# Kernel tuning notes

Hardware: AMD Instinct MI355X
Metric: run time of the kernel (lower is better)

## Reference

```python
import jax, jax.numpy as jnp
import numpy as np

B, T, N, D = 16, 64, 22, 64
K, E, DT, H = 4, 8, 5, 64
KL_WEIGHT = 0.01


def setup_inputs() -> dict:
    key = jax.random.key(0)
    ks = jax.random.split(key, 4)
    x = jax.random.normal(ks[0], (B, T, N, D), jnp.float32)
    # fixed-degree neighbor table: joint j's neighbors are (j..j+3) mod N, self first
    nb = jnp.asarray((np.arange(N)[:, None] + np.arange(K)[None, :]) % N, jnp.int32)
    Fin = DT * K * D  # 1280 flattened local window feature
    W1 = jax.random.normal(ks[1], (N, E, Fin, H), jnp.float32) / np.float32(np.sqrt(Fin))
    b1 = jnp.zeros((N, E, H), jnp.float32)
    W2 = jax.random.normal(ks[2], (N, E, H, H), jnp.float32) / np.float32(np.sqrt(H))
    b2 = jnp.zeros((N, E, H), jnp.float32)
    W3 = jax.random.normal(ks[3], (N, E, H, D), jnp.float32) / np.float32(np.sqrt(H))
    b3 = jnp.zeros((N, E, D), jnp.float32)
    return {"x": x, "nb": nb, "W1": W1, "b1": b1, "W2": W2, "b2": b2, "W3": W3, "b3": b3}


def reference(x, nb, W1, b1, W2, b2, W3, b3):
    Bx, Tx, Nx, Dx = x.shape
    dt_half = DT // 2
    # all valid centers t in range(dt_half, T - dt_half - 1), batched (no python loop over t, j)
    ts = jnp.arange(dt_half, Tx - dt_half - 1)            # [Tw]
    offs = jnp.arange(-dt_half, dt_half + 1)              # [DT]
    win = x[:, ts[:, None] + offs[None, :]]               # [B,Tw,DT,N,D]
    dx = win[:, :, :, nb, :]                              # [B,Tw,DT,N,K,D] neighbor gather
    Tw = ts.shape[0]
    f = dx.transpose(0, 1, 3, 2, 4, 5).reshape(Bx, Tw, Nx, DT * K * Dx)  # [B,Tw,N,Fin]
    # per-joint per-expert MLP, fully batched
    h = jax.nn.relu(jnp.einsum('btnf,nefh->btneh', f, W1) + b1)
    h = jax.nn.relu(jnp.einsum('btneh,nehg->btneg', h, W2) + b2)
    pred = jnp.einsum('btneh,nehd->btned', h, W3) + b3    # [B,Tw,N,E,D]
    y = x[:, ts]                                          # [B,Tw,N,D] center-frame target
    err = jnp.mean((pred - y[:, :, :, None, :]) ** 2, axis=-1)  # [B,Tw,N,E]
    min_err = jnp.min(err, axis=-1)                       # winner-take-all (monopoly)
    expert_idx_all = jnp.argmin(err, axis=-1)             # [B,Tw,N]
    p = jax.nn.softmax(-err, axis=-1)
    kl = jnp.sum(p * (jnp.log(p + 1e-9) + jnp.log(jnp.float32(E))), axis=-1)  # KL to uniform
    per_tj = jnp.mean(min_err + KL_WEIGHT * kl, axis=0)   # [Tw,N] batch-mean local losses
    # original divides by the FINAL loop indices j and t (off-by-one kept for fidelity)
    total = jnp.sum(per_tj) / jnp.float32(Nx - 1) / jnp.float32(Tx - dt_half - 2)
    expert_idx = expert_idx_all[:, -1, -1]                # last (t, j) iteration, [B]
    return total, expert_idx
```

## Files before the change

### kernel.cpp

```cpp
#include <hip/hip_runtime.h>
#include <math.h>

#define B_   16
#define T_   64
#define N_   22
#define D_   64
#define K_   4
#define E_   8
#define H_   64
#define TW   59
#define M_   (B_ * TW)
#define NE_  (N_ * E_)
#define NDXT (N_ * D_)
#define XTOT (B_ * T_ * N_ * D_)

typedef __attribute__((ext_vector_type(8))) short short8;
typedef __attribute__((ext_vector_type(4))) float float4v;

#define ERRWS_BYTES  ((size_t)(M_ * N_ * E_) * 4)
#define XH_OFF       (ERRWS_BYTES)

__device__ inline unsigned rtn_bf16(float f) {
    unsigned u = __float_as_uint(f);
    return (u + 0x7fffu + ((u >> 16) & 1u)) >> 16;
}

__global__ __launch_bounds__(256) void xtrunc_kernel(
    const float* __restrict__ x, short* __restrict__ xh, float* __restrict__ out)
{
    if (blockIdx.x == 0 && threadIdx.x == 0) out[0] = 0.f;
    int i = (blockIdx.x * 256 + threadIdx.x) * 4;
    if (i >= XTOT) return;
    float4 v = *(const float4*)(x + i);
    uint2 hp;
    hp.x = rtn_bf16(v.x) | (rtn_bf16(v.y) << 16);
    hp.y = rtn_bf16(v.z) | (rtn_bf16(v.w) << 16);
    *(uint2*)(xh + i) = hp;
}

__global__ __launch_bounds__(256, 4) void moe_err_kernel(
    const float* __restrict__ x, const short* __restrict__ xh,
    const int* __restrict__ nb,
    const float* __restrict__ W1, const float* __restrict__ W2,
    const float* __restrict__ W3,
    const float* __restrict__ b1, const float* __restrict__ b2,
    const float* __restrict__ b3, float* __restrict__ err_ws)
{
    const int tid = threadIdx.x;
    const int w   = tid >> 6;
    const int L   = tid & 63;
    const int g   = blockIdx.x;
    const int e   = g & 7;
    const int mt  = (g >> 3) & 7;
    const int n   = g >> 6;
    const int ne  = n * E_ + e;

    __shared__ __align__(16) char smem[26624];
    char*  wbuf   = smem;
    short* himg   = (short*)(smem + 8192);

    const int lrow = L & 15;
    const int dseg = (L >> 4) * 8;
    const int ccol = L & 15;
    const int qrow = (L >> 4) * 4;
    const int rowbase = mt * 128 + w * 32;

    const short* xhrow[2];
    #pragma unroll
    for (int rt = 0; rt < 2; ++rt) {
        int m  = rowbase + rt * 16 + lrow;
        int mc = m < M_ ? m : M_ - 1;
        int b = mc / TW, t = mc % TW;
        xhrow[rt] = xh + (size_t)(b * T_ + t) * NDXT;
    }

    const int o0 = __builtin_amdgcn_readfirstlane(nb[n * K_ + 0]) * D_;
    const int o1 = __builtin_amdgcn_readfirstlane(nb[n * K_ + 1]) * D_;
    const int o2 = __builtin_amdgcn_readfirstlane(nb[n * K_ + 2]) * D_;
    const int o3 = __builtin_amdgcn_readfirstlane(nb[n * K_ + 3]) * D_;

    const float* W1ne = W1 + (size_t)ne * (1280 * 64);
    const float* W2ne = W2 + (size_t)ne * 4096;
    const float* W3ne = W3 + (size_t)ne * 4096;
    auto csrc = [&](int c) {
        return c < 20 ? (W1ne + (size_t)c * 4096) : (c == 20 ? W2ne : W3ne);
    };

    float wf[2][2][8];
    uint4 wph[2];
    auto loadWf = [&](int wb, const float* src) {
        #pragma unroll
        for (int p = 0; p < 2; ++p) {
            const int pi = 2 * w + p;
            const float* sp = src + ((pi >> 2) * 32 + (L >> 4) * 8) * 64
                                  + ((pi & 3) * 16 + (L & 15));
            #pragma unroll
            for (int j = 0; j < 8; ++j) wf[wb][p][j] = sp[j * 64];
        }
    };
    auto packW = [&](int wb) {
        #pragma unroll
        for (int p = 0; p < 2; ++p) {
            unsigned hs[8];
            #pragma unroll
            for (int j = 0; j < 8; ++j) hs[j] = rtn_bf16(wf[wb][p][j]);
            wph[p].x = hs[0] | (hs[1] << 16); wph[p].y = hs[2] | (hs[3] << 16);
            wph[p].z = hs[4] | (hs[5] << 16); wph[p].w = hs[6] | (hs[7] << 16);
        }
    };
    auto storeW = [&]() {
        #pragma unroll
        for (int p = 0; p < 2; ++p) {
            *(uint4*)(wbuf + (size_t)(2 * w + p) * 1024 + (size_t)L * 16) = wph[p];
        }
    };
    auto bfrag = [&](int s2, int cf) -> short8 {
        return *(const short8*)(wbuf + (size_t)(s2 * 4 + cf) * 1024
                                     + (size_t)L * 16);
    };

    loadWf(0, csrc(0));
    loadWf(1, csrc(1));
    packW(0);

    float4v acc1[2][4];
    #pragma unroll
    for (int rt = 0; rt < 2; ++rt)
        #pragma unroll
        for (int cf = 0; cf < 4; ++cf) acc1[rt][cf] = (float4v)0.f;

    for (int dt = 0; dt < 5; ++dt) {
        #pragma unroll
        for (int kk = 0; kk < 4; ++kk) {
            const int c = dt * 4 + kk;
            __syncthreads();
            storeW();
            __syncthreads();

            loadWf(c & 1, csrc(c + 2));

            const int okk = (kk == 0) ? o0 : ((kk == 1) ? o1 : ((kk == 2) ? o2 : o3));
            const int off = dt * NDXT + okk;

            short8 ah[2][2];
            #pragma unroll
            for (int s2 = 0; s2 < 2; ++s2)
                #pragma unroll
                for (int rt = 0; rt < 2; ++rt)
                    ah[s2][rt] = *(const short8*)(xhrow[rt] + off + s2 * 32 + dseg);

            #pragma unroll
            for (int s2 = 0; s2 < 2; ++s2)
                #pragma unroll
                for (int cf = 0; cf < 4; ++cf) {
                    short8 bh = bfrag(s2, cf);
                    #pragma unroll
                    for (int rt = 0; rt < 2; ++rt)
                        acc1[rt][cf] = __builtin_amdgcn_mfma_f32_16x16x32_bf16(ah[s2][rt], bh, acc1[rt][cf], 0, 0, 0);
                }
            packW((c + 1) & 1);
        }
    }

    __syncthreads();
    storeW();
    #pragma unroll
    for (int cf = 0; cf < 4; ++cf) {
        float bv = b1[(size_t)ne * H_ + cf * 16 + ccol];
        #pragma unroll
        for (int rt = 0; rt < 2; ++rt)
            #pragma unroll
            for (int reg = 0; reg < 4; ++reg) {
                float hv = fmaxf(acc1[rt][cf][reg] + bv, 0.f);
                himg[(w * 32 + rt * 16 + qrow + reg) * 72 + cf * 16 + ccol] =
                    (short)rtn_bf16(hv);
            }
    }
    __syncthreads();

    float4v acc2[2][4];
    #pragma unroll
    for (int rt = 0; rt < 2; ++rt)
        #pragma unroll
        for (int cf = 0; cf < 4; ++cf) acc2[rt][cf] = (float4v)0.f;
    #pragma unroll
    for (int s2 = 0; s2 < 2; ++s2) {
        short8 ha[2];
        #pragma unroll
        for (int rt = 0; rt < 2; ++rt)
            ha[rt] = *(const short8*)&himg[(w * 32 + rt * 16 + lrow) * 72 + s2 * 32 + dseg];
        #pragma unroll
        for (int cf = 0; cf < 4; ++cf) {
            short8 bh = bfrag(s2, cf);
            #pragma unroll
            for (int rt = 0; rt < 2; ++rt)
                acc2[rt][cf] = __builtin_amdgcn_mfma_f32_16x16x32_bf16(ha[rt], bh, acc2[rt][cf], 0, 0, 0);
        }
    }
    packW(1);

    __syncthreads();
    storeW();
    #pragma unroll
    for (int cf = 0; cf < 4; ++cf) {
        float bv = b2[(size_t)ne * H_ + cf * 16 + ccol];
        #pragma unroll
        for (int rt = 0; rt < 2; ++rt)
            #pragma unroll
            for (int reg = 0; reg < 4; ++reg) {
                float hv = fmaxf(acc2[rt][cf][reg] + bv, 0.f);
                himg[(w * 32 + rt * 16 + qrow + reg) * 72 + cf * 16 + ccol] =
                    (short)rtn_bf16(hv);
            }
    }
    __syncthreads();

    float4v acc3[2][4];
    #pragma unroll
    for (int rt = 0; rt < 2; ++rt)
        #pragma unroll
        for (int cf = 0; cf < 4; ++cf) acc3[rt][cf] = (float4v)0.f;
    #pragma unroll
    for (int s2 = 0; s2 < 2; ++s2) {
        short8 ha[2];
        #pragma unroll
        for (int rt = 0; rt < 2; ++rt)
            ha[rt] = *(const short8*)&himg[(w * 32 + rt * 16 + lrow) * 72 + s2 * 32 + dseg];
        #pragma unroll
        for (int cf = 0; cf < 4; ++cf) {
            short8 bh = bfrag(s2, cf);
            #pragma unroll
            for (int rt = 0; rt < 2; ++rt)
                acc3[rt][cf] = __builtin_amdgcn_mfma_f32_16x16x32_bf16(ha[rt], bh, acc3[rt][cf], 0, 0, 0);
        }
    }

    {
        float b3v[4];
        #pragma unroll
        for (int cf = 0; cf < 4; ++cf) b3v[cf] = b3[(size_t)ne * D_ + cf * 16 + ccol];

        #pragma unroll
        for (int rt = 0; rt < 2; ++rt) {
            #pragma unroll
            for (int reg = 0; reg < 4; ++reg) {
                const int m  = rowbase + rt * 16 + qrow + reg;
                const int mc = m < M_ ? m : M_ - 1;
                const int b = mc / TW, t = mc % TW;
                const float* yp = x + ((size_t)(b * T_ + t + 2) * N_ + n) * D_;
                float s = 0.f;
                #pragma unroll
                for (int cf = 0; cf < 4; ++cf) {
                    float d = acc3[rt][cf][reg] + b3v[cf] - yp[cf * 16 + ccol];
                    s += d * d;
                }
                s += __shfl_xor(s, 1);
                s += __shfl_xor(s, 2);
                s += __shfl_xor(s, 4);
                s += __shfl_xor(s, 8);
                if (ccol == 0 && m < M_) {
                    err_ws[((size_t)m * N_ + n) * E_ + e] = s * (1.f / 64.f);
                }
            }
        }
    }
}

__global__ __launch_bounds__(256) void fix_kernel(
    const float* __restrict__ x, const int* __restrict__ nb,
    const float* __restrict__ W1, const float* __restrict__ b1,
    const float* __restrict__ W2, const float* __restrict__ b2,
    const float* __restrict__ W3, const float* __restrict__ b3,
    float* __restrict__ err_ws)
{
    const int b = blockIdx.x >> 3;
    const int e = blockIdx.x & 7;
    const int n = N_ - 1;
    const int t = TW - 1;
    const int ne = n * E_ + e;
    const int j = threadIdx.x & 63;
    const int q = threadIdx.x >> 6;

    __shared__ float fbuf[1280];
    __shared__ float part[4][64];
    __shared__ float h1s[64];
    __shared__ float h2s[64];

    for (int i = threadIdx.x; i < 1280; i += 256) {
        int dt = i >> 8, r = i & 255;
        int k = r >> 6, d = r & 63;
        int nk = nb[n * K_ + k];
        fbuf[i] = x[(((size_t)(b * T_ + t + dt)) * N_ + nk) * D_ + d];
    }
    __syncthreads();

    const float* W1p = W1 + (size_t)ne * 1280 * 64;
    float s = 0.f;
    #pragma unroll 8
    for (int k = q * 320; k < q * 320 + 320; ++k) s += fbuf[k] * W1p[(size_t)k * 64 + j];
    part[q][j] = s;
    __syncthreads();
    if (q == 0)
        h1s[j] = fmaxf(part[0][j] + part[1][j] + part[2][j] + part[3][j]
                       + b1[(size_t)ne * H_ + j], 0.f);
    __syncthreads();

    const float* W2p = W2 + (size_t)ne * 4096;
    s = 0.f;
    #pragma unroll
    for (int k = q * 16; k < q * 16 + 16; ++k) s += h1s[k] * W2p[k * 64 + j];
    part[q][j] = s;
    __syncthreads();
    if (q == 0)
        h2s[j] = fmaxf(part[0][j] + part[1][j] + part[2][j] + part[3][j]
                       + b2[(size_t)ne * H_ + j], 0.f);
    __syncthreads();

    const float* W3p = W3 + (size_t)ne * 4096;
    s = 0.f;
    #pragma unroll
    for (int k = q * 16; k < q * 16 + 16; ++k) s += h2s[k] * W3p[k * 64 + j];
    part[q][j] = s;
    __syncthreads();
    if (q == 0) {
        float pred = part[0][j] + part[1][j] + part[2][j] + part[3][j]
                   + b3[(size_t)ne * D_ + j];
        float y = x[(((size_t)(b * T_ + t + 2)) * N_ + n) * D_ + j];
        float d = pred - y;
        float sq = d * d;
        sq += __shfl_xor(sq, 1);
        sq += __shfl_xor(sq, 2);
        sq += __shfl_xor(sq, 4);
        sq += __shfl_xor(sq, 8);
        sq += __shfl_xor(sq, 16);
        sq += __shfl_xor(sq, 32);
        if (j == 0) {
            int m = b * TW + t;
            err_ws[((size_t)m * N_ + n) * E_ + e] = sq * (1.f / 64.f);
        }
    }
}

__global__ __launch_bounds__(256) void moe_reduce_kernel(
    const float* __restrict__ err_ws, float* __restrict__ out)
{
    const int tid = threadIdx.x;
    const int idx = blockIdx.x * 256 + tid;
    float v = 0.f;
    if (idx < M_ * N_) {
        const int m = idx / N_, n = idx % N_;
        const float* ep = err_ws + (size_t)idx * E_;
        float ev[E_];
        float4 e0 = *(const float4*)ep;
        float4 e1 = *(const float4*)(ep + 4);
        ev[0] = e0.x; ev[1] = e0.y; ev[2] = e0.z; ev[3] = e0.w;
        ev[4] = e1.x; ev[5] = e1.y; ev[6] = e1.z; ev[7] = e1.w;
        float mn = ev[0];
        int am = 0;
        #pragma unroll
        for (int i = 1; i < E_; ++i) {
            if (ev[i] < mn) { mn = ev[i]; am = i; }
        }
        float p[E_];
        float Z = 0.f;
        #pragma unroll
        for (int i = 0; i < E_; ++i) { p[i] = expf(mn - ev[i]); Z += p[i]; }
        const float invZ = 1.f / Z;
        float kl = 0.f;
        #pragma unroll
        for (int i = 0; i < E_; ++i) {
            float q = p[i] * invZ;
            kl += q * (logf(q + 1e-9f) + 2.0794415416798357f);
        }
        v = mn + 0.01f * kl;
        const int t = m % TW, b = m / TW;
        if (t == TW - 1 && n == N_ - 1) out[1 + b] = (float)am;
    }
    __shared__ float sd[256];
    sd[tid] = v;
    __syncthreads();
    for (int s = 128; s > 0; s >>= 1) {
        if (tid < s) sd[tid] += sd[tid + s];
        __syncthreads();
    }
    if (tid == 0) atomicAdd(out, sd[0] * (1.f / 20160.f));
}

extern "C" void kernel_launch(void* const* d_in, const int* in_sizes, int n_in,
                              void* d_out, int out_size, void* d_ws, size_t ws_size,
                              hipStream_t stream)
{
    const float* x  = (const float*)d_in[0];
    const int*   nb = (const int*)d_in[1];
    const float* W1 = (const float*)d_in[2];
    const float* b1 = (const float*)d_in[3];
    const float* W2 = (const float*)d_in[4];
    const float* b2 = (const float*)d_in[5];
    const float* W3 = (const float*)d_in[6];
    const float* b3 = (const float*)d_in[7];
    float* out    = (float*)d_out;
    float* err_ws = (float*)d_ws;
    short* xh     = (short*)((char*)d_ws + XH_OFF);

    hipLaunchKernelGGL(xtrunc_kernel, dim3((XTOT / 4 + 255) / 256), dim3(256), 0, stream,
                       x, xh, out);
    hipLaunchKernelGGL(moe_err_kernel, dim3(NE_ * 8), dim3(256), 0, stream,
                       x, xh, nb, W1, W2, W3, b1, b2, b3, err_ws);
    hipLaunchKernelGGL(fix_kernel, dim3(B_ * E_), dim3(256), 0, stream,
                       x, nb, W1, b1, W2, b2, W3, b3, err_ws);
    const int nred = (M_ * N_ + 255) / 256;
    hipLaunchKernelGGL(moe_reduce_kernel, dim3(nred), dim3(256), 0, stream, err_ws, out);
}
```

Baseline: 204.7 us.

## Fuse fix and bf16 pre-pass, fold reduction into last block, prefetch A

Merges the bf16 conversion of x and the special-case fix computation into one pre-kernel, so the main kernel no longer overwrites that entry. The final softmax/KL reduction moves into the main kernel using an atomic counter, letting the last-finishing block do it. This cuts the launch count from four to two. The A-fragment global loads are double-buffered one step ahead of the MFMAs to hide latency. The tail reduction now runs on a single block, which serializes that work, and it uses the fast exp/log intrinsics.

```diff
diff --git a/kernel.cpp b/kernel.cpp
--- a/kernel.cpp
+++ b/kernel.cpp
@@ -11,31 +11,118 @@
 #define TW   59
 #define M_   (B_ * TW)
 #define NE_  (N_ * E_)
+#define GRID (NE_ * 8)
 #define NDXT (N_ * D_)
 #define XTOT (B_ * T_ * N_ * D_)
+#define NF4  (XTOT / 4)
 
 typedef __attribute__((ext_vector_type(8))) short short8;
 typedef __attribute__((ext_vector_type(4))) float float4v;
 
 #define ERRWS_BYTES  ((size_t)(M_ * N_ * E_) * 4)
 #define XH_OFF       (ERRWS_BYTES)
+#define XIMG_BYTES   ((size_t)XTOT * 2)
+#define CNT_OFF      (XH_OFF + XIMG_BYTES)
 
 __device__ inline unsigned rtn_bf16(float f) {
     unsigned u = __float_as_uint(f);
     return (u + 0x7fffu + ((u >> 16) & 1u)) >> 16;
 }
 
-__global__ __launch_bounds__(256) void xtrunc_kernel(
-    const float* __restrict__ x, short* __restrict__ xh, float* __restrict__ out)
+__global__ __launch_bounds__(256) void pre_kernel(
+    const float* __restrict__ x, const int* __restrict__ nb,
+    const float* __restrict__ W1, const float* __restrict__ b1,
+    const float* __restrict__ W2, const float* __restrict__ b2,
+    const float* __restrict__ W3, const float* __restrict__ b3,
+    float* __restrict__ err_ws, short* __restrict__ xh,
+    unsigned* __restrict__ cnt)
 {
-    if (blockIdx.x == 0 && threadIdx.x == 0) out[0] = 0.f;
-    int i = (blockIdx.x * 256 + threadIdx.x) * 4;
-    if (i >= XTOT) return;
-    float4 v = *(const float4*)(x + i);
-    uint2 hp;
-    hp.x = rtn_bf16(v.x) | (rtn_bf16(v.y) << 16);
-    hp.y = rtn_bf16(v.z) | (rtn_bf16(v.w) << 16);
-    *(uint2*)(xh + i) = hp;
+    const int g   = blockIdx.x;
+    const int tid = threadIdx.x;
+    __shared__ __align__(16) char smem[6656];
+
+    if (g < 128) {
+        const int b = g >> 3;
+        const int e = g & 7;
+        const int n = N_ - 1, t = TW - 1;
+        const int ne = n * E_ + e;
+        const int j = tid & 63;
+        const int q = tid >> 6;
+
+        float* fbuf = (float*)smem;
+        float (*part)[64] = (float(*)[64])(smem + 5120);
+        float* h1s = (float*)(smem + 6144);
+        float* h2s = (float*)(smem + 6400);
+
+        if (g == 0 && tid == 0) *cnt = 0u;
+
+        for (int i = tid; i < 1280; i += 256) {
+            int dt = i >> 8, r = i & 255;
+            int k = r >> 6, d = r & 63;
+            int nk = nb[n * K_ + k];
+            fbuf[i] = x[(((size_t)(b * T_ + t + dt)) * N_ + nk) * D_ + d];
+        }
+        __syncthreads();
+
+        const float* W1p = W1 + (size_t)ne * 1280 * 64;
+        float s = 0.f;
+        #pragma unroll 8
+        for (int k = q * 320; k < q * 320 + 320; ++k) s += fbuf[k] * W1p[(size_t)k * 64 + j];
+        part[q][j] = s;
+        __syncthreads();
+        if (q == 0)
+            h1s[j] = fmaxf(part[0][j] + part[1][j] + part[2][j] + part[3][j]
+                           + b1[(size_t)ne * H_ + j], 0.f);
+        __syncthreads();
+
+        const float* W2p = W2 + (size_t)ne * 4096;
+        s = 0.f;
+        #pragma unroll
+        for (int k = q * 16; k < q * 16 + 16; ++k) s += h1s[k] * W2p[k * 64 + j];
+        part[q][j] = s;
+        __syncthreads();
+        if (q == 0)
+            h2s[j] = fmaxf(part[0][j] + part[1][j] + part[2][j] + part[3][j]
+                           + b2[(size_t)ne * H_ + j], 0.f);
+        __syncthreads();
+
+        const float* W3p = W3 + (size_t)ne * 4096;
+        s = 0.f;
+        #pragma unroll
+        for (int k = q * 16; k < q * 16 + 16; ++k) s += h2s[k] * W3p[k * 64 + j];
+        part[q][j] = s;
+        __syncthreads();
+        if (q == 0) {
+            float pred = part[0][j] + part[1][j] + part[2][j] + part[3][j]
+                       + b3[(size_t)ne * D_ + j];
+            float y = x[(((size_t)(b * T_ + t + 2)) * N_ + n) * D_ + j];
+            float d = pred - y;
+            float sq = d * d;
+            sq += __shfl_xor(sq, 1);
+            sq += __shfl_xor(sq, 2);
+            sq += __shfl_xor(sq, 4);
+            sq += __shfl_xor(sq, 8);
+            sq += __shfl_xor(sq, 16);
+            sq += __shfl_xor(sq, 32);
+            if (j == 0) {
+                int m = b * TW + t;
+                err_ws[((size_t)m * N_ + n) * E_ + e] = sq * (1.f / 64.f);
+            }
+        }
+    } else {
+        int base = (g - 128) * 256 + tid;
+        #pragma unroll
+        for (int it = 0; it < 2; ++it) {
+            int i = base + it * (1280 * 256);
+            if (i < NF4) {
+                float4 v = *(const float4*)(x + (size_t)i * 4);
+                uint2 hp;
+                hp.x = rtn_bf16(v.x) | (rtn_bf16(v.y) << 16);
+                hp.y = rtn_bf16(v.z) | (rtn_bf16(v.w) << 16);
+                *(uint2*)(xh + (size_t)i * 4) = hp;
+            }
+        }
+    }
 }
 
 __global__ __launch_bounds__(256, 4) void moe_err_kernel(
@@ -44,7 +131,8 @@
     const float* __restrict__ W1, const float* __restrict__ W2,
     const float* __restrict__ W3,
     const float* __restrict__ b1, const float* __restrict__ b2,
-    const float* __restrict__ b3, float* __restrict__ err_ws)
+    const float* __restrict__ b3, float* __restrict__ err_ws,
+    unsigned* __restrict__ cnt, float* __restrict__ out)
 {
     const int tid = threadIdx.x;
     const int w   = tid >> 6;
@@ -56,8 +144,8 @@
     const int ne  = n * E_ + e;
 
     __shared__ __align__(16) char smem[26624];
-    char*  wbuf   = smem;
-    short* himg   = (short*)(smem + 8192);
+    char*  wbuf = smem;
+    short* himg = (short*)(smem + 8192);
 
     const int lrow = L & 15;
     const int dseg = (L >> 4) * 8;
@@ -110,17 +198,26 @@
     };
     auto storeW = [&]() {
         #pragma unroll
-        for (int p = 0; p < 2; ++p) {
+        for (int p = 0; p < 2; ++p)
             *(uint4*)(wbuf + (size_t)(2 * w + p) * 1024 + (size_t)L * 16) = wph[p];
-        }
     };
     auto bfrag = [&](int s2, int cf) -> short8 {
         return *(const short8*)(wbuf + (size_t)(s2 * 4 + cf) * 1024
                                      + (size_t)L * 16);
     };
 
+    short8 ahb[2][2][2];
+    auto loadA = [&](int off, int buf) {
+        #pragma unroll
+        for (int s2 = 0; s2 < 2; ++s2)
+            #pragma unroll
+            for (int rt = 0; rt < 2; ++rt)
+                ahb[buf][s2][rt] = *(const short8*)(xhrow[rt] + off + s2 * 32 + dseg);
+    };
+
     loadWf(0, csrc(0));
     loadWf(1, csrc(1));
+    loadA(o0, 0);
     packW(0);
 
     float4v acc1[2][4];
@@ -137,17 +234,12 @@
             storeW();
             __syncthreads();
 
-            loadWf(c & 1, csrc(c + 2));
-
-            const int okk = (kk == 0) ? o0 : ((kk == 1) ? o1 : ((kk == 2) ? o2 : o3));
-            const int off = dt * NDXT + okk;
-
-            short8 ah[2][2];
-            #pragma unroll
-            for (int s2 = 0; s2 < 2; ++s2)
-                #pragma unroll
-                for (int rt = 0; rt < 2; ++rt)
-                    ah[s2][rt] = *(const short8*)(xhrow[rt] + off + s2 * 32 + dseg);
+            loadWf(kk & 1, csrc(c + 2));
+            if (c < 19) {
+                const int dtn = (kk == 3) ? dt + 1 : dt;
+                const int okn = (kk == 0) ? o1 : ((kk == 1) ? o2 : ((kk == 2) ? o3 : o0));
+                loadA(dtn * NDXT + okn, (kk + 1) & 1);
+            }
 
             #pragma unroll
             for (int s2 = 0; s2 < 2; ++s2)
@@ -156,7 +248,7 @@
                     short8 bh = bfrag(s2, cf);
                     #pragma unroll
                     for (int rt = 0; rt < 2; ++rt)
-                        acc1[rt][cf] = __builtin_amdgcn_mfma_f32_16x16x32_bf16(ah[s2][rt], bh, acc1[rt][cf], 0, 0, 0);
+                        acc1[rt][cf] = __builtin_amdgcn_mfma_f32_16x16x32_bf16(ahb[kk & 1][s2][rt], bh, acc1[rt][cf], 0, 0, 0);
                 }
             packW((c + 1) & 1);
         }
@@ -258,132 +350,61 @@
                 s += __shfl_xor(s, 2);
                 s += __shfl_xor(s, 4);
                 s += __shfl_xor(s, 8);
-                if (ccol == 0 && m < M_) {
+                if (ccol == 0 && m < M_ && !(n == N_ - 1 && t == TW - 1)) {
                     err_ws[((size_t)m * N_ + n) * E_ + e] = s * (1.f / 64.f);
                 }
             }
         }
     }
-}
-
-__global__ __launch_bounds__(256) void fix_kernel(
-    const float* __restrict__ x, const int* __restrict__ nb,
-    const float* __restrict__ W1, const float* __restrict__ b1,
-    const float* __restrict__ W2, const float* __restrict__ b2,
-    const float* __restrict__ W3, const float* __restrict__ b3,
-    float* __restrict__ err_ws)
-{
-    const int b = blockIdx.x >> 3;
-    const int e = blockIdx.x & 7;
-    const int n = N_ - 1;
-    const int t = TW - 1;
-    const int ne = n * E_ + e;
-    const int j = threadIdx.x & 63;
-    const int q = threadIdx.x >> 6;
-
-    __shared__ float fbuf[1280];
-    __shared__ float part[4][64];
-    __shared__ float h1s[64];
-    __shared__ float h2s[64];
-
-    for (int i = threadIdx.x; i < 1280; i += 256) {
-        int dt = i >> 8, r = i & 255;
-        int k = r >> 6, d = r & 63;
-        int nk = nb[n * K_ + k];
-        fbuf[i] = x[(((size_t)(b * T_ + t + dt)) * N_ + nk) * D_ + d];
-    }
-    __syncthreads();
-
-    const float* W1p = W1 + (size_t)ne * 1280 * 64;
-    float s = 0.f;
-    #pragma unroll 8
-    for (int k = q * 320; k < q * 320 + 320; ++k) s += fbuf[k] * W1p[(size_t)k * 64 + j];
-    part[q][j] = s;
-    __syncthreads();
-    if (q == 0)
-        h1s[j] = fmaxf(part[0][j] + part[1][j] + part[2][j] + part[3][j]
-                       + b1[(size_t)ne * H_ + j], 0.f);
-    __syncthreads();
-
-    const float* W2p = W2 + (size_t)ne * 4096;
-    s = 0.f;
-    #pragma unroll
-    for (int k = q * 16; k < q * 16 + 16; ++k) s += h1s[k] * W2p[k * 64 + j];
-    part[q][j] = s;
-    __syncthreads();
-    if (q == 0)
-        h2s[j] = fmaxf(part[0][j] + part[1][j] + part[2][j] + part[3][j]
-                       + b2[(size_t)ne * H_ + j], 0.f);
-    __syncthreads();
-
-    const float* W3p = W3 + (size_t)ne * 4096;
-    s = 0.f;
-    #pragma unroll
-    for (int k = q * 16; k < q * 16 + 16; ++k) s += h2s[k] * W3p[k * 64 + j];
-    part[q][j] = s;
-    __syncthreads();
-    if (q == 0) {
-        float pred = part[0][j] + part[1][j] + part[2][j] + part[3][j]
-                   + b3[(size_t)ne * D_ + j];
-        float y = x[(((size_t)(b * T_ + t + 2)) * N_ + n) * D_ + j];
-        float d = pred - y;
-        float sq = d * d;
-        sq += __shfl_xor(sq, 1);
-        sq += __shfl_xor(sq, 2);
-        sq += __shfl_xor(sq, 4);
-        sq += __shfl_xor(sq, 8);
-        sq += __shfl_xor(sq, 16);
-        sq += __shfl_xor(sq, 32);
-        if (j == 0) {
-            int m = b * TW + t;
-            err_ws[((size_t)m * N_ + n) * E_ + e] = sq * (1.f / 64.f);
-        }
-    }
-}
-
-__global__ __launch_bounds__(256) void moe_reduce_kernel(
-    const float* __restrict__ err_ws, float* __restrict__ out)
-{
-    const int tid = threadIdx.x;
-    const int idx = blockIdx.x * 256 + tid;
-    float v = 0.f;
-    if (idx < M_ * N_) {
-        const int m = idx / N_, n = idx % N_;
-        const float* ep = err_ws + (size_t)idx * E_;
-        float ev[E_];
-        float4 e0 = *(const float4*)ep;
-        float4 e1 = *(const float4*)(ep + 4);
-        ev[0] = e0.x; ev[1] = e0.y; ev[2] = e0.z; ev[3] = e0.w;
-        ev[4] = e1.x; ev[5] = e1.y; ev[6] = e1.z; ev[7] = e1.w;
-        float mn = ev[0];
-        int am = 0;
-        #pragma unroll
-        for (int i = 1; i < E_; ++i) {
-            if (ev[i] < mn) { mn = ev[i]; am = i; }
-        }
-        float p[E_];
-        float Z = 0.f;
-        #pragma unroll
-        for (int i = 0; i < E_; ++i) { p[i] = expf(mn - ev[i]); Z += p[i]; }
-        const float invZ = 1.f / Z;
-        float kl = 0.f;
-        #pragma unroll
-        for (int i = 0; i < E_; ++i) {
-            float q = p[i] * invZ;
-            kl += q * (logf(q + 1e-9f) + 2.0794415416798357f);
-        }
-        v = mn + 0.01f * kl;
-        const int t = m % TW, b = m / TW;
-        if (t == TW - 1 && n == N_ - 1) out[1 + b] = (float)am;
-    }
-    __shared__ float sd[256];
-    sd[tid] = v;
-    __syncthreads();
-    for (int s = 128; s > 0; s >>= 1) {
-        if (tid < s) sd[tid] += sd[tid + s];
-        __syncthreads();
-    }
-    if (tid == 0) atomicAdd(out, sd[0] * (1.f / 20160.f));
+
+    __syncthreads();
+    if (tid == 0) {
+        __threadfence();
+        unsigned old = atomicAdd(cnt, 1u);
+        *(int*)(smem + 1024) = (old == (unsigned)(GRID - 1)) ? 1 : 0;
+    }
+    __syncthreads();
+    if (*(int*)(smem + 1024)) {
+        __threadfence();
+        float partial = 0.f;
+        for (int idx = tid; idx < M_ * N_; idx += 256) {
+            const int m = idx / N_, nn = idx % N_;
+            const float* ep = err_ws + (size_t)idx * E_;
+            float ev[E_];
+            float4 e0 = *(const float4*)ep;
+            float4 e1 = *(const float4*)(ep + 4);
+            ev[0] = e0.x; ev[1] = e0.y; ev[2] = e0.z; ev[3] = e0.w;
+            ev[4] = e1.x; ev[5] = e1.y; ev[6] = e1.z; ev[7] = e1.w;
+            float mn = ev[0];
+            int am = 0;
+            #pragma unroll
+            for (int i = 1; i < E_; ++i) {
+                if (ev[i] < mn) { mn = ev[i]; am = i; }
+            }
+            float p[E_];
+            float Z = 0.f;
+            #pragma unroll
+            for (int i = 0; i < E_; ++i) { p[i] = __expf(mn - ev[i]); Z += p[i]; }
+            const float invZ = 1.f / Z;
+            float kl = 0.f;
+            #pragma unroll
+            for (int i = 0; i < E_; ++i) {
+                float q = p[i] * invZ;
+                kl += q * (__logf(q + 1e-9f) + 2.0794415416798357f);
+            }
+            partial += mn + 0.01f * kl;
+            const int t = m % TW, b = m / TW;
+            if (t == TW - 1 && nn == N_ - 1) out[1 + b] = (float)am;
+        }
+        float* sd = (float*)smem;
+        sd[tid] = partial;
+        __syncthreads();
+        for (int s = 128; s > 0; s >>= 1) {
+            if (tid < s) sd[tid] += sd[tid + s];
+            __syncthreads();
+        }
+        if (tid == 0) out[0] = sd[0] * (1.f / 20160.f);
+    }
 }
 
 extern "C" void kernel_launch(void* const* d_in, const int* in_sizes, int n_in,
@@ -401,13 +422,10 @@
     float* out    = (float*)d_out;
     float* err_ws = (float*)d_ws;
     short* xh     = (short*)((char*)d_ws + XH_OFF);
-
-    hipLaunchKernelGGL(xtrunc_kernel, dim3((XTOT / 4 + 255) / 256), dim3(256), 0, stream,
-                       x, xh, out);
-    hipLaunchKernelGGL(moe_err_kernel, dim3(NE_ * 8), dim3(256), 0, stream,
-                       x, xh, nb, W1, W2, W3, b1, b2, b3, err_ws);
-    hipLaunchKernelGGL(fix_kernel, dim3(B_ * E_), dim3(256), 0, stream,
-                       x, nb, W1, b1, W2, b2, W3, b3, err_ws);
-    const int nred = (M_ * N_ + 255) / 256;
-    hipLaunchKernelGGL(moe_reduce_kernel, dim3(nred), dim3(256), 0, stream, err_ws, out);
+    unsigned* cnt = (unsigned*)((char*)d_ws + CNT_OFF);
+
+    hipLaunchKernelGGL(pre_kernel, dim3(GRID), dim3(256), 0, stream,
+                       x, nb, W1, b1, W2, b2, W3, b3, err_ws, xh, cnt);
+    hipLaunchKernelGGL(moe_err_kernel, dim3(GRID), dim3(256), 0, stream,
+                       x, xh, nb, W1, W2, W3, b1, b2, b3, err_ws, cnt, out);
 }
```

Result: slower. 318.3 us (+55.5%).

## Fuse fp32 fix-up and bf16 conversion into one pre-kernel, raise occupancy

Applied to the files above, without the earlier changes.

Merges the separate bf16 truncation kernel and the fp32 fix-up kernel for the last (t, n) position into a single pre-kernel. The first 128 blocks do the fp32 fix-up and the remaining blocks convert x to bf16 with two elements per thread. The main MoE kernel now skips writing the fix-up entries, so ordering between the two kernels no longer matters. This removes one launch and lets the fix-up run beside the conversion instead of after the main kernel. Launch bounds on the main kernel are raised from 4 to 6 waves, which can cause register pressure or spills.

```diff
diff --git a/kernel.cpp b/kernel.cpp
--- a/kernel.cpp
+++ b/kernel.cpp
@@ -11,8 +11,10 @@
 #define TW   59
 #define M_   (B_ * TW)
 #define NE_  (N_ * E_)
+#define GRID (NE_ * 8)
 #define NDXT (N_ * D_)
 #define XTOT (B_ * T_ * N_ * D_)
+#define NF4  (XTOT / 4)
 
 typedef __attribute__((ext_vector_type(8))) short short8;
 typedef __attribute__((ext_vector_type(4))) float float4v;
@@ -25,20 +27,103 @@
     return (u + 0x7fffu + ((u >> 16) & 1u)) >> 16;
 }
 
-__global__ __launch_bounds__(256) void xtrunc_kernel(
-    const float* __restrict__ x, short* __restrict__ xh, float* __restrict__ out)
+__global__ __launch_bounds__(256) void pre_kernel(
+    const float* __restrict__ x, const int* __restrict__ nb,
+    const float* __restrict__ W1, const float* __restrict__ b1,
+    const float* __restrict__ W2, const float* __restrict__ b2,
+    const float* __restrict__ W3, const float* __restrict__ b3,
+    float* __restrict__ err_ws, short* __restrict__ xh,
+    float* __restrict__ out)
 {
-    if (blockIdx.x == 0 && threadIdx.x == 0) out[0] = 0.f;
-    int i = (blockIdx.x * 256 + threadIdx.x) * 4;
-    if (i >= XTOT) return;
-    float4 v = *(const float4*)(x + i);
-    uint2 hp;
-    hp.x = rtn_bf16(v.x) | (rtn_bf16(v.y) << 16);
-    hp.y = rtn_bf16(v.z) | (rtn_bf16(v.w) << 16);
-    *(uint2*)(xh + i) = hp;
+    const int g   = blockIdx.x;
+    const int tid = threadIdx.x;
+    __shared__ __align__(16) char smem[6656];
+
+    if (g < 128) {
+        const int b = g >> 3;
+        const int e = g & 7;
+        const int n = N_ - 1, t = TW - 1;
+        const int ne = n * E_ + e;
+        const int j = tid & 63;
+        const int q = tid >> 6;
+
+        float* fbuf = (float*)smem;
+        float (*part)[64] = (float(*)[64])(smem + 5120);
+        float* h1s = (float*)(smem + 6144);
+        float* h2s = (float*)(smem + 6400);
+
+        if (g == 0 && tid == 0) out[0] = 0.f;
+
+        for (int i = tid; i < 1280; i += 256) {
+            int dt = i >> 8, r = i & 255;
+            int k = r >> 6, d = r & 63;
+            int nk = nb[n * K_ + k];
+            fbuf[i] = x[(((size_t)(b * T_ + t + dt)) * N_ + nk) * D_ + d];
+        }
+        __syncthreads();
+
+        const float* W1p = W1 + (size_t)ne * 1280 * 64;
+        float s = 0.f;
+        #pragma unroll 8
+        for (int k = q * 320; k < q * 320 + 320; ++k) s += fbuf[k] * W1p[(size_t)k * 64 + j];
+        part[q][j] = s;
+        __syncthreads();
+        if (q == 0)
+            h1s[j] = fmaxf(part[0][j] + part[1][j] + part[2][j] + part[3][j]
+                           + b1[(size_t)ne * H_ + j], 0.f);
+        __syncthreads();
+
+        const float* W2p = W2 + (size_t)ne * 4096;
+        s = 0.f;
+        #pragma unroll
+        for (int k = q * 16; k < q * 16 + 16; ++k) s += h1s[k] * W2p[k * 64 + j];
+        part[q][j] = s;
+        __syncthreads();
+        if (q == 0)
+            h2s[j] = fmaxf(part[0][j] + part[1][j] + part[2][j] + part[3][j]
+                           + b2[(size_t)ne * H_ + j], 0.f);
+        __syncthreads();
+
+        const float* W3p = W3 + (size_t)ne * 4096;
+        s = 0.f;
+        #pragma unroll
+        for (int k = q * 16; k < q * 16 + 16; ++k) s += h2s[k] * W3p[k * 64 + j];
+        part[q][j] = s;
+        __syncthreads();
+        if (q == 0) {
+            float pred = part[0][j] + part[1][j] + part[2][j] + part[3][j]
+                       + b3[(size_t)ne * D_ + j];
+            float y = x[(((size_t)(b * T_ + t + 2)) * N_ + n) * D_ + j];
+            float d = pred - y;
+            float sq = d * d;
+            sq += __shfl_xor(sq, 1);
+            sq += __shfl_xor(sq, 2);
+            sq += __shfl_xor(sq, 4);
+            sq += __shfl_xor(sq, 8);
+            sq += __shfl_xor(sq, 16);
+            sq += __shfl_xor(sq, 32);
+            if (j == 0) {
+                int m = b * TW + t;
+                err_ws[((size_t)m * N_ + n) * E_ + e] = sq * (1.f / 64.f);
+            }
+        }
+    } else {
+        int base = (g - 128) * 256 + tid;
+        #pragma unroll
+        for (int it = 0; it < 2; ++it) {
+            int i = base + it * (1280 * 256);
+            if (i < NF4) {
+                float4 v = *(const float4*)(x + (size_t)i * 4);
+                uint2 hp;
+                hp.x = rtn_bf16(v.x) | (rtn_bf16(v.y) << 16);
+                hp.y = rtn_bf16(v.z) | (rtn_bf16(v.w) << 16);
+                *(uint2*)(xh + (size_t)i * 4) = hp;
+            }
+        }
+    }
 }
 
-__global__ __launch_bounds__(256, 4) void moe_err_kernel(
+__global__ __launch_bounds__(256, 6) void moe_err_kernel(
     const float* __restrict__ x, const short* __restrict__ xh,
     const int* __restrict__ nb,
     const float* __restrict__ W1, const float* __restrict__ W2,
@@ -56,8 +141,8 @@
     const int ne  = n * E_ + e;
 
     __shared__ __align__(16) char smem[26624];
-    char*  wbuf   = smem;
-    short* himg   = (short*)(smem + 8192);
+    char*  wbuf = smem;
+    short* himg = (short*)(smem + 8192);
 
     const int lrow = L & 15;
     const int dseg = (L >> 4) * 8;
@@ -110,9 +195,8 @@
     };
     auto storeW = [&]() {
         #pragma unroll
-        for (int p = 0; p < 2; ++p) {
+        for (int p = 0; p < 2; ++p)
             *(uint4*)(wbuf + (size_t)(2 * w + p) * 1024 + (size_t)L * 16) = wph[p];
-        }
     };
     auto bfrag = [&](int s2, int cf) -> short8 {
         return *(const short8*)(wbuf + (size_t)(s2 * 4 + cf) * 1024
@@ -258,85 +342,10 @@
                 s += __shfl_xor(s, 2);
                 s += __shfl_xor(s, 4);
                 s += __shfl_xor(s, 8);
-                if (ccol == 0 && m < M_) {
+                if (ccol == 0 && m < M_ && !(n == N_ - 1 && t == TW - 1)) {
                     err_ws[((size_t)m * N_ + n) * E_ + e] = s * (1.f / 64.f);
                 }
             }
-        }
-    }
-}
-
-__global__ __launch_bounds__(256) void fix_kernel(
-    const float* __restrict__ x, const int* __restrict__ nb,
-    const float* __restrict__ W1, const float* __restrict__ b1,
-    const float* __restrict__ W2, const float* __restrict__ b2,
-    const float* __restrict__ W3, const float* __restrict__ b3,
-    float* __restrict__ err_ws)
-{
-    const int b = blockIdx.x >> 3;
-    const int e = blockIdx.x & 7;
-    const int n = N_ - 1;
-    const int t = TW - 1;
-    const int ne = n * E_ + e;
-    const int j = threadIdx.x & 63;
-    const int q = threadIdx.x >> 6;
-
-    __shared__ float fbuf[1280];
-    __shared__ float part[4][64];
-    __shared__ float h1s[64];
-    __shared__ float h2s[64];
-
-    for (int i = threadIdx.x; i < 1280; i += 256) {
-        int dt = i >> 8, r = i & 255;
-        int k = r >> 6, d = r & 63;
-        int nk = nb[n * K_ + k];
-        fbuf[i] = x[(((size_t)(b * T_ + t + dt)) * N_ + nk) * D_ + d];
-    }
-    __syncthreads();
-
-    const float* W1p = W1 + (size_t)ne * 1280 * 64;
-    float s = 0.f;
-    #pragma unroll 8
-    for (int k = q * 320; k < q * 320 + 320; ++k) s += fbuf[k] * W1p[(size_t)k * 64 + j];
-    part[q][j] = s;
-    __syncthreads();
-    if (q == 0)
-        h1s[j] = fmaxf(part[0][j] + part[1][j] + part[2][j] + part[3][j]
-                       + b1[(size_t)ne * H_ + j], 0.f);
-    __syncthreads();
-
-    const float* W2p = W2 + (size_t)ne * 4096;
-    s = 0.f;
-    #pragma unroll
-    for (int k = q * 16; k < q * 16 + 16; ++k) s += h1s[k] * W2p[k * 64 + j];
-    part[q][j] = s;
-    __syncthreads();
-    if (q == 0)
-        h2s[j] = fmaxf(part[0][j] + part[1][j] + part[2][j] + part[3][j]
-                       + b2[(size_t)ne * H_ + j], 0.f);
-    __syncthreads();
-
-    const float* W3p = W3 + (size_t)ne * 4096;
-    s = 0.f;
-    #pragma unroll
-    for (int k = q * 16; k < q * 16 + 16; ++k) s += h2s[k] * W3p[k * 64 + j];
-    part[q][j] = s;
-    __syncthreads();
-    if (q == 0) {
-        float pred = part[0][j] + part[1][j] + part[2][j] + part[3][j]
-                   + b3[(size_t)ne * D_ + j];
-        float y = x[(((size_t)(b * T_ + t + 2)) * N_ + n) * D_ + j];
-        float d = pred - y;
-        float sq = d * d;
-        sq += __shfl_xor(sq, 1);
-        sq += __shfl_xor(sq, 2);
-        sq += __shfl_xor(sq, 4);
-        sq += __shfl_xor(sq, 8);
-        sq += __shfl_xor(sq, 16);
-        sq += __shfl_xor(sq, 32);
-        if (j == 0) {
-            int m = b * TW + t;
-            err_ws[((size_t)m * N_ + n) * E_ + e] = sq * (1.f / 64.f);
         }
     }
 }
@@ -402,12 +411,10 @@
     float* err_ws = (float*)d_ws;
     short* xh     = (short*)((char*)d_ws + XH_OFF);
 
-    hipLaunchKernelGGL(xtrunc_kernel, dim3((XTOT / 4 + 255) / 256), dim3(256), 0, stream,
-                       x, xh, out);
-    hipLaunchKernelGGL(moe_err_kernel, dim3(NE_ * 8), dim3(256), 0, stream,
+    hipLaunchKernelGGL(pre_kernel, dim3(GRID), dim3(256), 0, stream,
+                       x, nb, W1, b1, W2, b2, W3, b3, err_ws, xh, out);
+    hipLaunchKernelGGL(moe_err_kernel, dim3(GRID), dim3(256), 0, stream,
                        x, xh, nb, W1, W2, W3, b1, b2, b3, err_ws);
-    hipLaunchKernelGGL(fix_kernel, dim3(B_ * E_), dim3(256), 0, stream,
-                       x, nb, W1, b1, W2, b2, W3, b3, err_ws);
     const int nred = (M_ * N_ + 255) / 256;
     hipLaunchKernelGGL(moe_reduce_kernel, dim3(nred), dim3(256), 0, stream, err_ws, out);
 }
```

Measured after the change: 335.8 us. +64.0%, slower.
